# Performance work log

Hardware: AMD Instinct MI355X
Metric: run time of the kernel (lower is better)

The kernel has to match this reference:

```python
import jax, jax.numpy as jnp
import numpy as np

B, N, M = 8, 1024, 1024
DIM2 = 1280          # config.dim * 2
KIN = 1344           # esm_dim + cell_line_dim
H, DK = 8, 64        # heads, attn_dim_key
SCALE = DK ** -0.5


def setup_inputs() -> dict:
    key = jax.random.key(0)
    ks = jax.random.split(key, 7)
    rna_reps = jax.random.normal(ks[0], (B, N, DIM2), dtype=jnp.float32)
    protein_reps = jax.random.normal(ks[1], (B, M, KIN), dtype=jnp.float32)
    # learned params (Linear stores weight [out, in])
    Wq = jax.random.normal(ks[2], (H * DK, DIM2), dtype=jnp.float32) * (DIM2 ** -0.5)
    bq = jnp.zeros((H * DK,), dtype=jnp.float32)
    Wk = jax.random.normal(ks[3], (H * DK, KIN), dtype=jnp.float32) * (KIN ** -0.5)
    bk = jnp.zeros((H * DK,), dtype=jnp.float32)
    rel_bias = jax.random.normal(ks[4], (1, H, 1, DK), dtype=jnp.float32)
    return {"rna_reps": rna_reps, "protein_reps": protein_reps,
            "Wq": Wq, "bq": bq, "Wk": Wk, "bk": bk, "rel_bias": rel_bias}


def reference(rna_reps, protein_reps, Wq, bq, Wk, bk, rel_bias):
    b = rna_reps.shape[0]
    q = rna_reps @ Wq.T + bq           # [b, n, h*dk]
    k = protein_reps @ Wk.T + bk       # [b, m, h*dk]
    q = q.reshape(b, N, H, DK).transpose(0, 2, 1, 3)   # b h n d
    k = k.reshape(b, M, H, DK).transpose(0, 2, 1, 3)   # b h m d
    q = q * SCALE
    logits = jnp.einsum('bhid,bhjd->bhij', q + rel_bias, k)  # [b,h,n,m]
    out = jnp.mean(logits, axis=1)     # mean over heads -> [b,n,m]
    # dropout p=0.0 (eval) -> identity
    return out
```

## Files before the change

kernel.cpp:

```cpp
#include <hip/hip_runtime.h>
#include <hip/hip_bf16.h>


typedef __bf16 bf16x8 __attribute__((ext_vector_type(8)));
typedef __bf16 bf16x4 __attribute__((ext_vector_type(4)));
typedef float f32x4 __attribute__((ext_vector_type(4)));

__device__ inline bf16x4 cvt4(const f32x4 a) {
    bf16x4 r;
    r[0] = (__bf16)a[0]; r[1] = (__bf16)a[1];
    r[2] = (__bf16)a[2]; r[3] = (__bf16)a[3];
    return r;
}

__device__ inline void gload4(f32x4& dst, const float* p) {
    asm volatile("global_load_dwordx4 %0, %1, off"
                 : "=&v"(dst) : "v"(p) : "memory");
}

__global__ __launch_bounds__(256, 2)
void proj_all(const float* __restrict__ rna,  const float* __restrict__ prot,
              const float* __restrict__ Wq,   const float* __restrict__ bq,
              const float* __restrict__ Wk,   const float* __restrict__ bk,
              const float* __restrict__ rb,
              __bf16* __restrict__ qout, __bf16* __restrict__ kout)
{
    __shared__ __bf16 AS[2][128 * 64];
    __shared__ __bf16 WS[2][128 * 64];

    const int bid = blockIdx.x;
    const int wg  = (bid & 7) * 64 + (bid >> 3);
    const bool isQ = wg < 256;
    const int lwg  = isQ ? wg : wg - 256;
    const int brow = (lwg >> 2) * 128;
    const int bcol = (lwg & 3) * 128;

    const float* A    = isQ ? rna : prot;
    const float* W    = isQ ? Wq  : Wk;
    const float* bias = isQ ? bq  : bk;
    __bf16*      out  = isQ ? qout : kout;
    const int    K    = isQ ? 1280 : 1344;
    const int    nt   = K >> 6;

    const int tid  = threadIdx.x;
    const int lane = tid & 63;
    const int wid  = tid >> 6;
    const int wr   = wid >> 1;
    const int wc   = wid & 1;
    const int fr   = lane & 15;
    const int q4   = lane >> 4;

    const int rloc = wid * 32 + q4;
    const float* aGlob = A + (size_t)(brow + rloc) * K + fr * 4;
    const float* wGlob = W + (size_t)(bcol + rloc) * K + fr * 4;
    const int lb = rloc * 128 + (((fr >> 1) ^ (q4 << 1)) << 4) + (lane & 1) * 8;
    const int rmask = ((fr & 3) << 1) | ((fr >> 2) & 1);

    f32x4 acc[4][4] = {};
    f32x4 a0[8], a1[8], wv[8];

#define ISSUE_A(k0, ra) do {                                              \
    _Pragma("unroll")                                                     \
    for (int i_ = 0; i_ < 8; ++i_)                                        \
        gload4(ra[i_], aGlob + (size_t)(i_ * 4) * K + (k0));              \
    } while (0)

#define ISSUE_W(k0) do {                                                  \
    _Pragma("unroll")                                                     \
    for (int i_ = 0; i_ < 8; ++i_)                                        \
        gload4(wv[i_], wGlob + (size_t)(i_ * 4) * K + (k0));              \
    } while (0)

#define STAGE(p, ra) do {                                                 \
    char* as_ = (char*)AS[p]; char* ws_ = (char*)WS[p];                   \
    _Pragma("unroll")                                                     \
    for (int i_ = 0; i_ < 8; ++i_) {                                      \
        *(bf16x4*)(as_ + ((lb ^ ((i_ & 1) << 4)) + i_ * 512)) = cvt4(ra[i_]); \
        *(bf16x4*)(ws_ + ((lb ^ ((i_ & 1) << 4)) + i_ * 512)) = cvt4(wv[i_]); \
    } } while (0)

#define COMPUTE(p) do {                                                   \
    const char* as_ = (const char*)AS[p];                                 \
    const char* ws_ = (const char*)WS[p];                                 \
    _Pragma("unroll")                                                     \
    for (int kk_ = 0; kk_ < 2; ++kk_) {                                   \
        bf16x8 af[4], bw[4];                                              \
        _Pragma("unroll")                                                 \
        for (int m_ = 0; m_ < 4; ++m_)                                    \
            af[m_] = *(const bf16x8*)(as_ + (wr * 64 + m_ * 16 + fr) * 128 \
                                          + (((kk_ * 4 + q4) ^ rmask) << 4)); \
        _Pragma("unroll")                                                 \
        for (int n_ = 0; n_ < 4; ++n_)                                    \
            bw[n_] = *(const bf16x8*)(ws_ + (wc * 64 + n_ * 16 + fr) * 128 \
                                          + (((kk_ * 4 + q4) ^ rmask) << 4)); \
        _Pragma("unroll")                                                 \
        for (int m_ = 0; m_ < 4; ++m_)                                    \
            _Pragma("unroll")                                             \
            for (int n_ = 0; n_ < 4; ++n_)                                \
                acc[m_][n_] = __builtin_amdgcn_mfma_f32_16x16x32_bf16(    \
                    af[m_], bw[n_], acc[m_][n_], 0, 0, 0);                \
    } } while (0)

#define STEP(t, p, ra) do {                                               \
    if ((t) + 1 < nt) asm volatile("s_waitcnt vmcnt(8)" ::: "memory");    \
    else              asm volatile("s_waitcnt vmcnt(0)" ::: "memory");    \
    __builtin_amdgcn_sched_barrier(0);        \
    STAGE(p, ra);                                                         \
    __builtin_amdgcn_sched_barrier(0);                                    \
    if ((t) + 1 < nt) ISSUE_W(((t) + 1) * 64);                            \
    if ((t) + 2 < nt) ISSUE_A(((t) + 2) * 64, ra);                        \
    __builtin_amdgcn_sched_barrier(0);                                    \
    asm volatile("s_waitcnt lgkmcnt(0)" ::: "memory");    \
    __builtin_amdgcn_s_barrier();          \
    __builtin_amdgcn_sched_barrier(0);                                    \
    COMPUTE(p);                                                           \
} while (0)

    ISSUE_A(0, a0);
    ISSUE_W(0);
    ISSUE_A(64, a1);

    int t = 0;
    for (; t + 1 < nt; t += 2) {
        STEP(t,     0, a0);
        STEP(t + 1, 1, a1);
    }
    if (t < nt) STEP(t, 0, a0);

#undef ISSUE_A
#undef ISSUE_W
#undef STAGE
#undef COMPUTE
#undef STEP

    const int r0 = (lane >> 4) * 4;
    #pragma unroll
    for (int n = 0; n < 4; ++n) {
        const int c = bcol + wc * 64 + n * 16 + fr;
        const float bv = bias[c];
        const float rv = isQ ? rb[c] : 0.0f;
        #pragma unroll
        for (int m = 0; m < 4; ++m) {
            const int row = brow + wr * 64 + m * 16 + r0;
            #pragma unroll
            for (int j = 0; j < 4; ++j) {
                float v = acc[m][n][j] + bv;
                if (isQ) v = 0.125f * v + rv;
                out[(size_t)(row + j) * 512 + c] = (__bf16)v;
            }
        }
    }
}

__global__ __launch_bounds__(256, 2)
void attn_kernel(const __bf16* __restrict__ Q,
                 const __bf16* __restrict__ Kb,
                 float* __restrict__ out)
{
    __shared__ __bf16 As[128 * 64];
    __shared__ __bf16 Bs[128 * 64];

    const int tid  = threadIdx.x;
    const int lane = tid & 63;
    const int wid  = tid >> 6;
    const int wr   = wid >> 1;
    const int wc   = wid & 1;
    const int b    = blockIdx.z;
    const int brow = blockIdx.y * 128;
    const int bcol = blockIdx.x * 128;

    const __bf16* Qb = Q  + (size_t)b * 1024 * 512;
    const __bf16* Kp = Kb + (size_t)b * 1024 * 512;

    const int fr = lane & 15;
    const int q4 = lane >> 4;

    f32x4 acc[4][4] = {};

    const int lr3 = lane >> 3;
    const int m3  = ((lr3 & 3) << 1) | ((lr3 >> 2) & 1);
    const int scol = ((lane & 7) ^ m3) * 8;
    const int rmask = ((fr & 3) << 1) | ((fr >> 2) & 1);

    for (int k0 = 0; k0 < 512; k0 += 64) {
        __syncthreads();
        #pragma unroll
        for (int i = 0; i < 4; ++i) {
            const int rbase = wid * 32 + i * 8;
            const __bf16* sa = Qb + (size_t)(brow + rbase + lr3) * 512 + k0 + scol;
            const __bf16* sb = Kp + (size_t)(bcol + rbase + lr3) * 512 + k0 + scol;
            __builtin_amdgcn_global_load_lds(
                (const __attribute__((address_space(1))) void*)sa,
                (__attribute__((address_space(3))) void*)&As[rbase * 64], 16, 0, 0);
            __builtin_amdgcn_global_load_lds(
                (const __attribute__((address_space(1))) void*)sb,
                (__attribute__((address_space(3))) void*)&Bs[rbase * 64], 16, 0, 0);
        }
        __syncthreads();

        #pragma unroll
        for (int kk = 0; kk < 2; ++kk) {
            const int ci = kk * 4 + q4;
            bf16x8 af[4], bf_[4];
            #pragma unroll
            for (int m = 0; m < 4; ++m)
                af[m] = *(const bf16x8*)(&As[(wr * 64 + m * 16 + fr) * 64 + ((ci ^ rmask) << 3)]);
            #pragma unroll
            for (int n = 0; n < 4; ++n)
                bf_[n] = *(const bf16x8*)(&Bs[(wc * 64 + n * 16 + fr) * 64 + ((ci ^ rmask) << 3)]);
            #pragma unroll
            for (int m = 0; m < 4; ++m)
                #pragma unroll
                for (int n = 0; n < 4; ++n)
                    acc[m][n] = __builtin_amdgcn_mfma_f32_16x16x32_bf16(af[m], bf_[n], acc[m][n], 0, 0, 0);
        }
    }

    float* op = out + (size_t)b * 1024 * 1024;
    const int r0 = (lane >> 4) * 4;
    #pragma unroll
    for (int n = 0; n < 4; ++n) {
        const int col = bcol + wc * 64 + n * 16 + fr;
        #pragma unroll
        for (int m = 0; m < 4; ++m) {
            const int row = brow + wr * 64 + m * 16 + r0;
            #pragma unroll
            for (int j = 0; j < 4; ++j)
                op[(size_t)(row + j) * 1024 + col] = 0.125f * acc[m][n][j];
        }
    }
}

extern "C" void kernel_launch(void* const* d_in, const int* in_sizes, int n_in,
                              void* d_out, int out_size, void* d_ws, size_t ws_size,
                              hipStream_t stream) {
    const float* rna  = (const float*)d_in[0];
    const float* prot = (const float*)d_in[1];
    const float* Wq   = (const float*)d_in[2];
    const float* bq   = (const float*)d_in[3];
    const float* Wk   = (const float*)d_in[4];
    const float* bk   = (const float*)d_in[5];
    const float* rb   = (const float*)d_in[6];

    __bf16* qws = (__bf16*)d_ws;
    __bf16* kws = qws + (size_t)8192 * 512;

    proj_all<<<dim3(512), dim3(256), 0, stream>>>(rna, prot, Wq, bq, Wk, bk, rb, qws, kws);
    attn_kernel<<<dim3(8, 8, 8), dim3(256), 0, stream>>>(qws, kws, (float*)d_out);
}
```

Baseline: 60.19 us.

## Restructure projection GEMM pipeline to stage next tile during current compute

Reorganizes the software pipeline of the projection GEMM. Each step now writes the next tile into the other LDS buffer and issues the global loads for the tile after that before running MFMAs on the current buffer, so there is one barrier per step instead of a barrier between staging and compute. It drops the separate A register buffers (a0/a1) in favour of a single av/wv set, which lowers register pressure. It also raises wave priority around the MFMA block. The cost is a full vmcnt(0) wait at the start of each step, which may expose more global-load latency.

```diff
diff --git a/kernel.cpp b/kernel.cpp
--- a/kernel.cpp
+++ b/kernel.cpp
@@ -57,31 +57,29 @@
     const int rmask = ((fr & 3) << 1) | ((fr >> 2) & 1);
 
     f32x4 acc[4][4] = {};
-    f32x4 a0[8], a1[8], wv[8];
-
-#define ISSUE_A(k0, ra) do {                                              \
+    f32x4 av[8], wv[8];
+
+#define ISSUE_ALL(k0) do {                                                \
     _Pragma("unroll")                                                     \
     for (int i_ = 0; i_ < 8; ++i_)                                        \
-        gload4(ra[i_], aGlob + (size_t)(i_ * 4) * K + (k0));              \
-    } while (0)
-
-#define ISSUE_W(k0) do {                                                  \
+        gload4(av[i_], aGlob + (size_t)(i_ * 4) * K + (k0));              \
     _Pragma("unroll")                                                     \
     for (int i_ = 0; i_ < 8; ++i_)                                        \
         gload4(wv[i_], wGlob + (size_t)(i_ * 4) * K + (k0));              \
     } while (0)
 
-#define STAGE(p, ra) do {                                                 \
+#define STAGE(p) do {                                                     \
     char* as_ = (char*)AS[p]; char* ws_ = (char*)WS[p];                   \
     _Pragma("unroll")                                                     \
     for (int i_ = 0; i_ < 8; ++i_) {                                      \
-        *(bf16x4*)(as_ + ((lb ^ ((i_ & 1) << 4)) + i_ * 512)) = cvt4(ra[i_]); \
+        *(bf16x4*)(as_ + ((lb ^ ((i_ & 1) << 4)) + i_ * 512)) = cvt4(av[i_]); \
         *(bf16x4*)(ws_ + ((lb ^ ((i_ & 1) << 4)) + i_ * 512)) = cvt4(wv[i_]); \
     } } while (0)
 
 #define COMPUTE(p) do {                                                   \
     const char* as_ = (const char*)AS[p];                                 \
     const char* ws_ = (const char*)WS[p];                                 \
+    __builtin_amdgcn_s_setprio(1);                                        \
     _Pragma("unroll")                                                     \
     for (int kk_ = 0; kk_ < 2; ++kk_) {                                   \
         bf16x8 af[4], bw[4];                                              \
@@ -99,36 +97,37 @@
             for (int n_ = 0; n_ < 4; ++n_)                                \
                 acc[m_][n_] = __builtin_amdgcn_mfma_f32_16x16x32_bf16(    \
                     af[m_], bw[n_], acc[m_][n_], 0, 0, 0);                \
-    } } while (0)
-
-#define STEP(t, p, ra) do {                                               \
-    if ((t) + 1 < nt) asm volatile("s_waitcnt vmcnt(8)" ::: "memory");    \
-    else              asm volatile("s_waitcnt vmcnt(0)" ::: "memory");    \
+    }                                                                     \
+    __builtin_amdgcn_s_setprio(0);                                        \
+    } while (0)
+
+#define STEP(t, p) do {                                                   \
+    asm volatile("s_waitcnt vmcnt(0)" ::: "memory");                      \
     __builtin_amdgcn_sched_barrier(0);        \
-    STAGE(p, ra);                                                         \
+    if ((t) + 1 < nt) STAGE((p) ^ 1);                                     \
+    if ((t) + 2 < nt) ISSUE_ALL(((t) + 2) * 64);                          \
+    COMPUTE(p);                                                           \
+    asm volatile("s_waitcnt lgkmcnt(0)" ::: "memory");                    \
+    __builtin_amdgcn_s_barrier();                                         \
     __builtin_amdgcn_sched_barrier(0);                                    \
-    if ((t) + 1 < nt) ISSUE_W(((t) + 1) * 64);                            \
-    if ((t) + 2 < nt) ISSUE_A(((t) + 2) * 64, ra);                        \
-    __builtin_amdgcn_sched_barrier(0);                                    \
-    asm volatile("s_waitcnt lgkmcnt(0)" ::: "memory");    \
-    __builtin_amdgcn_s_barrier();          \
-    __builtin_amdgcn_sched_barrier(0);                                    \
-    COMPUTE(p);                                                           \
 } while (0)
 
-    ISSUE_A(0, a0);
-    ISSUE_W(0);
-    ISSUE_A(64, a1);
-
-    int t = 0;
-    for (; t + 1 < nt; t += 2) {
-        STEP(t,     0, a0);
-        STEP(t + 1, 1, a1);
-    }
-    if (t < nt) STEP(t, 0, a0);
-
-#undef ISSUE_A
-#undef ISSUE_W
+    ISSUE_ALL(0);
+    asm volatile("s_waitcnt vmcnt(0)" ::: "memory");
+    __builtin_amdgcn_sched_barrier(0);
+    STAGE(0);
+    ISSUE_ALL(64);
+    asm volatile("s_waitcnt lgkmcnt(0)" ::: "memory");
+    __builtin_amdgcn_s_barrier();
+    __builtin_amdgcn_sched_barrier(0);
+
+    for (int t = 0; t + 1 < nt; t += 2) {
+        STEP(t, 0);
+        STEP(t + 1, 1);
+    }
+    if (nt & 1) STEP(nt - 1, 0);
+
+#undef ISSUE_ALL
 #undef STAGE
 #undef COMPUTE
 #undef STEP
```

Result: faster. 58.40 us (-3.0%).
